# Optimization experiments

Measured on AMD Instinct MI355X. Metric: run time of the kernel, lower is better.

Reference implementation:

```python
import jax, jax.numpy as jnp
import numpy as np

B, T, K, D, H, HL, S, KN = 4096, 50, 32, 64, 256, 128, 100000, 1000


def setup_inputs() -> dict:
    key = jax.random.key(0)
    ks = jax.random.split(key, 24)
    inp = {
        "uididx": jax.random.randint(ks[0], (B,), 0, S, dtype=jnp.int32),
        "kcodeidx": jax.random.randint(ks[1], (B, K), 0, KN, dtype=jnp.int32),
        "kcode_len": jax.random.randint(ks[2], (B,), 1, K + 1, dtype=jnp.int32),
        "qidemb": jax.random.normal(ks[3], (B, T, D), dtype=jnp.float32),
        "qid_len": jax.random.randint(ks[4], (B,), 1, T + 1, dtype=jnp.int32),
        # embedding tables
        "stuE": jax.random.normal(ks[5], (S, D), dtype=jnp.float32) * 0.1,
        "knE": jax.random.normal(ks[6], (KN, D), dtype=jnp.float32) * 0.1,
        # Theta DNN params
        "T_W1": jax.random.normal(ks[7], (D, H), dtype=jnp.float32) * (1.0 / np.sqrt(D)),
        "T_b1": jnp.zeros((H,), jnp.float32),
        "T_W2": jax.random.normal(ks[8], (H, 1), dtype=jnp.float32) * (1.0 / np.sqrt(H)),
        "T_b2": jnp.zeros((1,), jnp.float32),
        # A DNN params
        "A_W1": jax.random.normal(ks[9], (D, H), dtype=jnp.float32) * (1.0 / np.sqrt(D)),
        "A_b1": jnp.zeros((H,), jnp.float32),
        "A_W2": jax.random.normal(ks[10], (H, 1), dtype=jnp.float32) * (1.0 / np.sqrt(H)),
        "A_b2": jnp.zeros((1,), jnp.float32),
        # LSTM params (gate order i,f,g,o) + output head
        "L_Wi": jax.random.normal(ks[11], (D, 4 * HL), dtype=jnp.float32) * (1.0 / np.sqrt(D)),
        "L_Wh": jax.random.normal(ks[12], (HL, 4 * HL), dtype=jnp.float32) * (1.0 / np.sqrt(HL)),
        "L_b": jnp.zeros((4 * HL,), jnp.float32),
        "L_Wo": jax.random.normal(ks[13], (HL, 1), dtype=jnp.float32) * (1.0 / np.sqrt(HL)),
        "L_bo": jnp.zeros((1,), jnp.float32),
    }
    return inp


def _dnn(x, W1, b1, W2, b2):
    return jnp.tanh(x @ W1 + b1) @ W2 + b2


def _lstm_last(x, lengths, Wi, Wh, b):
    # x: [B,T,D]; returns last valid hidden state [B,HL]
    xg = jnp.einsum('btd,dh->bth', x, Wi) + b  # precomputed input projections
    h0 = jnp.zeros((x.shape[0], Wh.shape[0]), x.dtype)

    def step(carry, inp):
        h, c = carry
        g_x, t = inp
        g = g_x + h @ Wh
        i, f, gg, o = jnp.split(g, 4, axis=-1)
        c2 = jax.nn.sigmoid(f) * c + jax.nn.sigmoid(i) * jnp.tanh(gg)
        h2 = jax.nn.sigmoid(o) * jnp.tanh(c2)
        upd = (t < lengths)[:, None]
        return (jnp.where(upd, h2, h), jnp.where(upd, c2, c)), None

    (h, _), _ = jax.lax.scan(step, (h0, h0), (xg.transpose(1, 0, 2), jnp.arange(x.shape[1])))
    return h


def reference(uididx, kcodeidx, kcode_len, qidemb, qid_len, stuE, knE,
              T_W1, T_b1, T_W2, T_b2, A_W1, A_b1, A_W2, A_b2,
              L_Wi, L_Wh, L_b, L_Wo, L_bo):
    stu = stuE[uididx]            # [B,D]
    kemb = knE[kcodeidx]          # [B,K,D]
    kmask = jnp.arange(kcodeidx.shape[1])[None, :] < kcode_len[:, None]  # [B,K]
    kmf = kmask.astype(kemb.dtype)

    # per-student mastery: sigmoid(kemb @ stu / 5), then masked reductions
    mastery = jax.nn.sigmoid(jnp.einsum('bkd,bd->bk', kemb, stu) / 5.0)
    mastvec = jnp.einsum('bk,bkd->bd', mastery * kmf, kemb)  # sum(mastery * kemb)
    avec = jnp.einsum('bk,bkd->bd', kmf, kemb)               # sum(kemb)

    # scaled dot-product attention: q=qidemb, k=v=kemb, scale=0.15
    scores = jnp.einsum('btd,bkd->btk', qidemb, kemb) * 0.15
    scores = jnp.where(kmask[:, None, :], scores, -1e9)
    attw = jax.nn.softmax(scores, axis=-1)
    bvec = jnp.einsum('btk,bkd->btd', attw, kemb)            # [B,T,D]

    t = _dnn(mastvec, T_W1, T_b1, T_W2, T_b2)                             # theta [B,1]
    a = 8.0 * (jax.nn.sigmoid(jnp.abs(_dnn(avec, A_W1, A_b1, A_W2, A_b2))) - 0.5)
    hT = _lstm_last(bvec, qid_len, L_Wi, L_Wh, L_b)
    b = 8.0 * (jax.nn.sigmoid(hT @ L_Wo + L_bo) - 0.5)                    # [B,1]

    return jax.nn.sigmoid(a * (t - b))  # IRT response probability [B,1]
```

## Files before the change

### kernel.cpp

```cpp
#include <hip/hip_runtime.h>
#include <math.h>

#define B_  4096
#define T_  50
#define K_  32
#define D_  64
#define H_  256
#define HL_ 128
#define G4_ 512

typedef __attribute__((ext_vector_type(8))) short bf16x8;
typedef __attribute__((ext_vector_type(4))) float f32x4;

__device__ __forceinline__ float fast_exp(float x){ return __expf(x); }
__device__ __forceinline__ float fast_rcp(float x){ return __builtin_amdgcn_rcpf(x); }
__device__ __forceinline__ float sigmoidf_(float x){ return fast_rcp(1.f + fast_exp(-x)); }
__device__ __forceinline__ float tanhf_(float x){ return 1.f - 2.f*fast_rcp(1.f + fast_exp(2.f*x)); }

__device__ __forceinline__ short f2bf(float f){
  union { float f; unsigned u; } v; v.f = f;
  unsigned r = v.u + 0x7FFFu + ((v.u >> 16) & 1u);
  return (short)(r >> 16);
}
__device__ __forceinline__ float bf2f(short s){
  union { unsigned u; float f; } v; v.u = ((unsigned)(unsigned short)s) << 16;
  return v.f;
}

__device__ __forceinline__ float wave_reduce_sum(float v){
  #pragma unroll
  for (int off = 32; off; off >>= 1) v += __shfl_xor(v, off);
  return v;
}

#define KROW 72
#define PROW 40

__global__ __launch_bounds__(256) void head_kernel(
    const int* __restrict__ uididx, const int* __restrict__ kcodeidx,
    const int* __restrict__ kcode_len, const float* __restrict__ qidemb,
    const int* __restrict__ qid_len, const float* __restrict__ stuE,
    const float* __restrict__ knE,
    const float* __restrict__ T_W1, const float* __restrict__ T_b1,
    const float* __restrict__ T_W2, const float* __restrict__ T_b2,
    const float* __restrict__ A_W1, const float* __restrict__ A_b1,
    const float* __restrict__ A_W2, const float* __restrict__ A_b2,
    short* __restrict__ bvec, float* __restrict__ t_val, float* __restrict__ a_val)
{
  __shared__ __align__(16) short s_kemb[K_*KROW];
  __shared__ __align__(16) short s_kembT[D_*PROW];
  __shared__ __align__(16) short s_p[64*PROW];
  __shared__ float s_stu[D_];
  __shared__ float s_mast[K_];
  __shared__ float s_kmf[K_];
  __shared__ float s_mvec[D_];
  __shared__ float s_avec[D_];
  __shared__ float s_redT[4];
  __shared__ float s_redA[4];

  const int b    = blockIdx.x;
  const int tid  = threadIdx.x;
  const int lane = tid & 63;
  const int w    = tid >> 6;
  const int l15  = lane & 15;
  const int quad = lane >> 4;
  const int klen = kcode_len[b];
  const int qlen = qid_len[b];

  if (tid < D_) s_stu[tid] = stuE[uididx[b]*D_ + tid];
  #pragma unroll
  for (int i = tid; i < 512; i += 256){
    int k = i >> 4, f4 = i & 15;
    const float4 v = *(const float4*)&knE[(size_t)kcodeidx[b*K_ + k]*D_ + f4*4];
    short4 b4; b4.x = f2bf(v.x); b4.y = f2bf(v.y); b4.z = f2bf(v.z); b4.w = f2bf(v.w);
    *(short4*)&s_kemb[k*KROW + f4*4] = b4;
    int d = f4*4;
    s_kembT[(d+0)*PROW + k] = b4.x;
    s_kembT[(d+1)*PROW + k] = b4.y;
    s_kembT[(d+2)*PROW + k] = b4.z;
    s_kembT[(d+3)*PROW + k] = b4.w;
  }
  __syncthreads();

  {
    int k = tid >> 3, l8 = tid & 7;
    float s = 0.f;
    #pragma unroll
    for (int j = 0; j < 8; ++j){
      int d = l8 + 8*((j + k) & 7);
      s += s_stu[d] * bf2f(s_kemb[k*KROW + d]);
    }
    s += __shfl_xor(s, 1); s += __shfl_xor(s, 2); s += __shfl_xor(s, 4);
    if (l8 == 0){
      float valid = (k < klen) ? 1.f : 0.f;
      s_mast[k] = valid * sigmoidf_(s * 0.2f);
      s_kmf[k]  = valid;
    }
  }
  __syncthreads();

  if (tid < D_){
    float mv = 0.f, av = 0.f;
    #pragma unroll 4
    for (int k = 0; k < K_; ++k){
      float e = bf2f(s_kemb[k*KROW + tid]);
      mv += s_mast[k] * e;
      av += s_kmf[k]  * e;
    }
    s_mvec[tid] = mv; s_avec[tid] = av;
  }
  __syncthreads();

  {
    const int qrow = w*16 + l15;
    bf16x8 aq[2];
    #pragma unroll
    for (int kt = 0; kt < 2; ++kt){
      if (qrow < qlen){
        const float4 v0 = *(const float4*)&qidemb[((size_t)b*T_ + qrow)*D_ + kt*32 + quad*8];
        const float4 v1 = *(const float4*)&qidemb[((size_t)b*T_ + qrow)*D_ + kt*32 + quad*8 + 4];
        aq[kt][0]=f2bf(v0.x); aq[kt][1]=f2bf(v0.y); aq[kt][2]=f2bf(v0.z); aq[kt][3]=f2bf(v0.w);
        aq[kt][4]=f2bf(v1.x); aq[kt][5]=f2bf(v1.y); aq[kt][6]=f2bf(v1.z); aq[kt][7]=f2bf(v1.w);
      } else {
        aq[kt][0]=0; aq[kt][1]=0; aq[kt][2]=0; aq[kt][3]=0;
        aq[kt][4]=0; aq[kt][5]=0; aq[kt][6]=0; aq[kt][7]=0;
      }
    }
    f32x4 zero = {0.f, 0.f, 0.f, 0.f};
    f32x4 accs[2] = {zero, zero};
    #pragma unroll
    for (int kt = 0; kt < 2; ++kt){
      #pragma unroll
      for (int nt = 0; nt < 2; ++nt){
        bf16x8 bk = *(const bf16x8*)&s_kemb[(nt*16 + l15)*KROW + kt*32 + quad*8];
        accs[nt] = __builtin_amdgcn_mfma_f32_16x16x32_bf16(aq[kt], bk, accs[nt], 0, 0, 0);
      }
    }
    #pragma unroll
    for (int r = 0; r < 4; ++r){
      float v0 = (l15      < klen) ? accs[0][r]*0.15f : -1e9f;
      float v1 = (l15 + 16 < klen) ? accs[1][r]*0.15f : -1e9f;
      float mx = fmaxf(v0, v1);
      #pragma unroll
      for (int off = 1; off < 16; off <<= 1) mx = fmaxf(mx, __shfl_xor(mx, off));
      float e0 = fast_exp(v0 - mx), e1 = fast_exp(v1 - mx);
      float sm = e0 + e1;
      #pragma unroll
      for (int off = 1; off < 16; off <<= 1) sm += __shfl_xor(sm, off);
      float inv = fast_rcp(sm);
      int row = w*16 + quad*4 + r;
      s_p[row*PROW + l15]      = f2bf(e0 * inv);
      s_p[row*PROW + 16 + l15] = f2bf(e1 * inv);
    }
    bf16x8 ap = *(const bf16x8*)&s_p[(w*16 + l15)*PROW + quad*8];
    #pragma unroll
    for (int nt = 0; nt < 4; ++nt){
      bf16x8 bv = *(const bf16x8*)&s_kembT[(nt*16 + l15)*PROW + quad*8];
      f32x4 acco = __builtin_amdgcn_mfma_f32_16x16x32_bf16(ap, bv, zero, 0, 0, 0);
      #pragma unroll
      for (int r = 0; r < 4; ++r){
        int t = w*16 + quad*4 + r;
        if (t < qlen) bvec[((size_t)b*T_ + t)*D_ + nt*16 + l15] = f2bf(acco[r]);
      }
    }
  }

  {
    float accT = T_b1[tid];
    float accA = A_b1[tid];
    #pragma unroll 4
    for (int d = 0; d < D_; ++d){
      float mv = s_mvec[d], av = s_avec[d];
      accT += mv * T_W1[d*H_ + tid];
      accA += av * A_W1[d*H_ + tid];
    }
    float termT = tanhf_(accT) * T_W2[tid];
    float termA = tanhf_(accA) * A_W2[tid];
    termT = wave_reduce_sum(termT);
    termA = wave_reduce_sum(termA);
    if (lane == 0){ s_redT[w] = termT; s_redA[w] = termA; }
    __syncthreads();
    if (tid == 0){
      t_val[b] = s_redT[0] + s_redT[1] + s_redT[2] + s_redT[3] + T_b2[0];
      float v = s_redA[0] + s_redA[1] + s_redA[2] + s_redA[3] + A_b2[0];
      a_val[b] = 8.f * (sigmoidf_(fabsf(v)) - 0.5f);
    }
  }
}

#define AROW 408

__global__ __launch_bounds__(512, 2) void lstm_kernel(
    const short* __restrict__ bvec, const int* __restrict__ qid_len,
    const float* __restrict__ L_Wi, const float* __restrict__ L_Wh,
    const float* __restrict__ L_b,  const float* __restrict__ L_Wo,
    const float* __restrict__ L_bo, const float* __restrict__ t_val,
    const float* __restrict__ a_val, float* __restrict__ out)
{
  __shared__ __align__(16) short s_A[16*AROW];
  __shared__ int s_len[16];

  const int tid  = threadIdx.x;
  const int s0   = blockIdx.x * 16;
  const int w    = tid >> 6;
  const int lane = tid & 63;
  const int l15  = lane & 15;
  const int quad = lane >> 4;

  bf16x8 wf[4][6];
  float  biasv[4];
  #pragma unroll
  for (int g = 0; g < 4; ++g){
    const int col = g*128 + w*16 + l15;
    biasv[g] = L_b[col];
    #pragma unroll
    for (int kt = 0; kt < 6; ++kt){
      #pragma unroll
      for (int j = 0; j < 8; ++j){
        int k = kt*32 + quad*8 + j;
        float v = (k < D_) ? L_Wi[k*G4_ + col] : L_Wh[(k-D_)*G4_ + col];
        wf[g][kt][j] = f2bf(v);
      }
    }
  }

  for (int p = tid; p < 16*AROW; p += 512) s_A[p] = 0;
  if (tid < 16) s_len[tid] = qid_len[s0 + tid];
  __syncthreads();

  const int xs = tid >> 5, xpos = tid & 31;
  {
    const short2 xv = *(const short2*)&bvec[((size_t)(s0+xs)*T_ + 0)*D_ + xpos*2];
    *(short2*)&s_A[xs*AROW + xpos*2] = xv;
  }
  int maxlen = 0;
  int len_r[4];
  #pragma unroll
  for (int i = 0; i < 16; ++i) maxlen = max(maxlen, s_len[i]);
  #pragma unroll
  for (int r = 0; r < 4; ++r) len_r[r] = s_len[quad*4 + r];
  float c_reg[4] = {0.f,0.f,0.f,0.f};
  float h_reg[4] = {0.f,0.f,0.f,0.f};

  short2 xv_reg;
  if (1 < maxlen) xv_reg = *(const short2*)&bvec[((size_t)(s0+xs)*T_ + 1)*D_ + xpos*2];
  __syncthreads();

  for (int t = 0; t < maxlen; ++t){
    const int xb = t & 1;
    const int hb = xb ^ 1;
    if (t + 1 < maxlen) *(short2*)&s_A[xs*AROW + hb*64 + xpos*2] = xv_reg;
    if (t + 2 < maxlen)
      xv_reg = *(const short2*)&bvec[((size_t)(s0+xs)*T_ + (t+2))*D_ + xpos*2];

    bf16x8 af[6];
    af[0] = *(const bf16x8*)&s_A[l15*AROW + xb*64 +      quad*8];
    af[1] = *(const bf16x8*)&s_A[l15*AROW + xb*64 + 32 + quad*8];
    #pragma unroll
    for (int kt = 0; kt < 4; ++kt)
      af[2+kt] = *(const bf16x8*)&s_A[l15*AROW + 128 + hb*128 + kt*32 + quad*8];

    f32x4 acc[4];
    #pragma unroll
    for (int g = 0; g < 4; ++g){
      f32x4 a; a[0]=biasv[g]; a[1]=biasv[g]; a[2]=biasv[g]; a[3]=biasv[g];
      acc[g] = a;
    }
    #pragma unroll
    for (int kt = 0; kt < 6; ++kt){
      #pragma unroll
      for (int g = 0; g < 4; ++g)
        acc[g] = __builtin_amdgcn_mfma_f32_16x16x32_bf16(af[kt], wf[g][kt], acc[g], 0, 0, 0);
    }

    #pragma unroll
    for (int r = 0; r < 4; ++r){
      if (t < len_r[r]){
        float gi = acc[0][r], gf = acc[1][r], gg = acc[2][r], go = acc[3][r];
        float c2 = sigmoidf_(gf)*c_reg[r] + sigmoidf_(gi)*tanhf_(gg);
        float h2 = sigmoidf_(go)*tanhf_(c2);
        c_reg[r] = c2; h_reg[r] = h2;
      }
      s_A[(quad*4 + r)*AROW + 128 + xb*128 + w*16 + l15] = f2bf(h_reg[r]);
    }
    __syncthreads();
  }

  const int xbLast = (maxlen - 1) & 1;
  for (int s2 = w; s2 < 16; s2 += 8){
    float h0 = bf2f(s_A[s2*AROW + 128 + xbLast*128 + lane]);
    float h1 = bf2f(s_A[s2*AROW + 128 + xbLast*128 + 64 + lane]);
    float part = h0*L_Wo[lane] + h1*L_Wo[64+lane];
    part = wave_reduce_sum(part);
    if (lane == 0){
      float bb = 8.f * (sigmoidf_(part + L_bo[0]) - 0.5f);
      out[s0+s2] = sigmoidf_(a_val[s0+s2] * (t_val[s0+s2] - bb));
    }
  }
}

extern "C" void kernel_launch(void* const* d_in, const int* in_sizes, int n_in,
                              void* d_out, int out_size, void* d_ws, size_t ws_size,
                              hipStream_t stream)
{
  (void)in_sizes; (void)n_in; (void)out_size; (void)ws_size;
  const int*   uididx    = (const int*)  d_in[0];
  const int*   kcodeidx  = (const int*)  d_in[1];
  const int*   kcode_len = (const int*)  d_in[2];
  const float* qidemb    = (const float*)d_in[3];
  const int*   qid_len   = (const int*)  d_in[4];
  const float* stuE      = (const float*)d_in[5];
  const float* knE       = (const float*)d_in[6];
  const float* T_W1      = (const float*)d_in[7];
  const float* T_b1      = (const float*)d_in[8];
  const float* T_W2      = (const float*)d_in[9];
  const float* T_b2      = (const float*)d_in[10];
  const float* A_W1      = (const float*)d_in[11];
  const float* A_b1      = (const float*)d_in[12];
  const float* A_W2      = (const float*)d_in[13];
  const float* A_b2      = (const float*)d_in[14];
  const float* L_Wi      = (const float*)d_in[15];
  const float* L_Wh      = (const float*)d_in[16];
  const float* L_b       = (const float*)d_in[17];
  const float* L_Wo      = (const float*)d_in[18];
  const float* L_bo      = (const float*)d_in[19];
  float* out = (float*)d_out;

  short* bvec  = (short*)d_ws;
  float* t_val = (float*)(bvec + (size_t)B_*T_*D_);
  float* a_val = t_val + B_;

  hipLaunchKernelGGL(head_kernel, dim3(B_), dim3(256), 0, stream,
    uididx, kcodeidx, kcode_len, qidemb, qid_len, stuE, knE,
    T_W1, T_b1, T_W2, T_b2, A_W1, A_b1, A_W2, A_b2,
    bvec, t_val, a_val);

  hipLaunchKernelGGL(lstm_kernel, dim3(B_/16), dim3(512), 0, stream,
    bvec, qid_len, L_Wi, L_Wh, L_b, L_Wo, L_bo, t_val, a_val, out);
}
```

Before: 221.2 us.

## Transpose LSTM MFMA operands, pack h stores, unroll time loop by two

Swaps the MFMA operand order so each lane's accumulator holds four consecutive gate columns for one sample. This lets the hidden state be packed into one 8-byte LDS store per lane instead of four scalar stores, and the length mask becomes one per-lane comparison applied with selects instead of a branch. The time loop is unrolled by two so the double-buffer indices are compile-time constants. The launch-bounds occupancy hint of 2 is dropped, which lets the compiler use more registers at the risk of lower occupancy.

```diff
diff --git a/kernel.cpp b/kernel.cpp
--- a/kernel.cpp
+++ b/kernel.cpp
@@ -190,7 +190,7 @@
 
 #define AROW 408
 
-__global__ __launch_bounds__(512, 2) void lstm_kernel(
+__global__ __launch_bounds__(512) void lstm_kernel(
     const short* __restrict__ bvec, const int* __restrict__ qid_len,
     const float* __restrict__ L_Wi, const float* __restrict__ L_Wh,
     const float* __restrict__ L_b,  const float* __restrict__ L_Wo,
@@ -208,11 +208,12 @@
   const int quad = lane >> 4;
 
   bf16x8 wf[4][6];
-  float  biasv[4];
+  f32x4  biasv4[4];
   #pragma unroll
   for (int g = 0; g < 4; ++g){
     const int col = g*128 + w*16 + l15;
-    biasv[g] = L_b[col];
+    #pragma unroll
+    for (int r = 0; r < 4; ++r) biasv4[g][r] = L_b[g*128 + w*16 + quad*4 + r];
     #pragma unroll
     for (int kt = 0; kt < 6; ++kt){
       #pragma unroll
@@ -234,11 +235,9 @@
     *(short2*)&s_A[xs*AROW + xpos*2] = xv;
   }
   int maxlen = 0;
-  int len_r[4];
   #pragma unroll
   for (int i = 0; i < 16; ++i) maxlen = max(maxlen, s_len[i]);
-  #pragma unroll
-  for (int r = 0; r < 4; ++r) len_r[r] = s_len[quad*4 + r];
+  const int mylen = s_len[l15];
   float c_reg[4] = {0.f,0.f,0.f,0.f};
   float h_reg[4] = {0.f,0.f,0.f,0.f};
 
@@ -246,45 +245,50 @@
   if (1 < maxlen) xv_reg = *(const short2*)&bvec[((size_t)(s0+xs)*T_ + 1)*D_ + xpos*2];
   __syncthreads();
 
-  for (int t = 0; t < maxlen; ++t){
-    const int xb = t & 1;
-    const int hb = xb ^ 1;
-    if (t + 1 < maxlen) *(short2*)&s_A[xs*AROW + hb*64 + xpos*2] = xv_reg;
-    if (t + 2 < maxlen)
-      xv_reg = *(const short2*)&bvec[((size_t)(s0+xs)*T_ + (t+2))*D_ + xpos*2];
-
-    bf16x8 af[6];
-    af[0] = *(const bf16x8*)&s_A[l15*AROW + xb*64 +      quad*8];
-    af[1] = *(const bf16x8*)&s_A[l15*AROW + xb*64 + 32 + quad*8];
-    #pragma unroll
-    for (int kt = 0; kt < 4; ++kt)
-      af[2+kt] = *(const bf16x8*)&s_A[l15*AROW + 128 + hb*128 + kt*32 + quad*8];
-
-    f32x4 acc[4];
-    #pragma unroll
-    for (int g = 0; g < 4; ++g){
-      f32x4 a; a[0]=biasv[g]; a[1]=biasv[g]; a[2]=biasv[g]; a[3]=biasv[g];
-      acc[g] = a;
-    }
-    #pragma unroll
-    for (int kt = 0; kt < 6; ++kt){
-      #pragma unroll
-      for (int g = 0; g < 4; ++g)
-        acc[g] = __builtin_amdgcn_mfma_f32_16x16x32_bf16(af[kt], wf[g][kt], acc[g], 0, 0, 0);
-    }
-
-    #pragma unroll
-    for (int r = 0; r < 4; ++r){
-      if (t < len_r[r]){
-        float gi = acc[0][r], gf = acc[1][r], gg = acc[2][r], go = acc[3][r];
-        float c2 = sigmoidf_(gf)*c_reg[r] + sigmoidf_(gi)*tanhf_(gg);
-        float h2 = sigmoidf_(go)*tanhf_(c2);
-        c_reg[r] = c2; h_reg[r] = h2;
-      }
-      s_A[(quad*4 + r)*AROW + 128 + xb*128 + w*16 + l15] = f2bf(h_reg[r]);
-    }
-    __syncthreads();
-  }
+#define LSTM_STEP(TI, XB) do {                                                 \
+    const int xb_ = (XB); const int hb_ = xb_ ^ 1;                             \
+    if ((TI) + 1 < maxlen) *(short2*)&s_A[xs*AROW + hb_*64 + xpos*2] = xv_reg; \
+    if ((TI) + 2 < maxlen)                                                     \
+      xv_reg = *(const short2*)&bvec[((size_t)(s0+xs)*T_ + ((TI)+2))*D_ + xpos*2]; \
+    bf16x8 af[6];                                                              \
+    af[0] = *(const bf16x8*)&s_A[l15*AROW + xb_*64 +      quad*8];             \
+    af[1] = *(const bf16x8*)&s_A[l15*AROW + xb_*64 + 32 + quad*8];             \
+    _Pragma("unroll")                                                          \
+    for (int kt = 0; kt < 4; ++kt)                                             \
+      af[2+kt] = *(const bf16x8*)&s_A[l15*AROW + 128 + hb_*128 + kt*32 + quad*8]; \
+    f32x4 acc[4];                                                              \
+    acc[0]=biasv4[0]; acc[1]=biasv4[1]; acc[2]=biasv4[2]; acc[3]=biasv4[3];    \
+    _Pragma("unroll")                                                          \
+    for (int kt = 0; kt < 6; ++kt){                                            \
+      _Pragma("unroll")                                                        \
+      for (int g = 0; g < 4; ++g)                                              \
+        acc[g] = __builtin_amdgcn_mfma_f32_16x16x32_bf16(wf[g][kt], af[kt], acc[g], 0, 0, 0); \
+    }                                                                          \
+    const bool upd_ = (TI) < mylen;                                            \
+    _Pragma("unroll")                                                          \
+    for (int r = 0; r < 4; ++r){                                               \
+      float gi = acc[0][r], gf = acc[1][r], gg = acc[2][r], go = acc[3][r];    \
+      float c2 = sigmoidf_(gf)*c_reg[r] + sigmoidf_(gi)*tanhf_(gg);            \
+      float h2 = sigmoidf_(go)*tanhf_(c2);                                     \
+      c_reg[r] = upd_ ? c2 : c_reg[r];                                         \
+      h_reg[r] = upd_ ? h2 : h_reg[r];                                         \
+    }                                                                          \
+    uint2 hp_;                                                                 \
+    hp_.x = (unsigned)(unsigned short)f2bf(h_reg[0])                           \
+          | ((unsigned)(unsigned short)f2bf(h_reg[1]) << 16);                  \
+    hp_.y = (unsigned)(unsigned short)f2bf(h_reg[2])                           \
+          | ((unsigned)(unsigned short)f2bf(h_reg[3]) << 16);                  \
+    *(uint2*)&s_A[l15*AROW + 128 + xb_*128 + w*16 + quad*4] = hp_;             \
+    __syncthreads();                                                           \
+  } while(0)
+
+  int t = 0;
+  for (; t + 1 < maxlen; t += 2){
+    LSTM_STEP(t,   0);
+    LSTM_STEP(t+1, 1);
+  }
+  if (t < maxlen) LSTM_STEP(t, 0);
+#undef LSTM_STEP
 
   const int xbLast = (maxlen - 1) & 1;
   for (int s2 = w; s2 < 16; s2 += 8){
```

Result: no change. 221.8 us (+0.3%).
